# Kernel tuning notes

Hardware: AMD Instinct MI355X
Metric: run time of the kernel (lower is better)

## Reference

```python
import jax, jax.numpy as jnp
import numpy as np

KE = 14.3996454784255
P = 6  # polynomial cutoff order
A_EXP = 0.3
A_PREFACTOR = 0.4543
C = jnp.array([0.1818, 0.5099, 0.2802, 0.02817], dtype=jnp.float32)
K = jnp.array([3.2, 0.9423, 0.4028, 0.2016], dtype=jnp.float32)

N_NODES = 100000
N_EDGES = 6400000
N_ELEM = 10
N_RADII = 119


def setup_inputs() -> dict:
    key = jax.random.key(0)
    k1, k2, k3, k4, k5 = jax.random.split(key, 5)
    # edge distances in a physically plausible range (avoid x ~ 0 -> 1/x blowup)
    x = jax.random.uniform(k1, (N_EDGES, 1), dtype=jnp.float32) * 4.0 + 0.05
    node_attrs = jax.random.uniform(k2, (N_NODES, N_ELEM), dtype=jnp.float32)
    edge_index = jax.random.randint(k3, (2, N_EDGES), 0, N_NODES, dtype=jnp.int64)
    atomic_numbers = jax.random.randint(k4, (N_ELEM,), 1, N_RADII, dtype=jnp.int64)
    # covalent radii table (stand-in for ase.data.covalent_radii), ~0.3..2.6 Angstrom
    covalent_radii = 0.3 + 2.3 * jax.random.uniform(k5, (N_RADII,), dtype=jnp.float32)
    return {
        "x": x,
        "node_attrs": node_attrs,
        "edge_index": edge_index,
        "atomic_numbers": atomic_numbers,
        "covalent_radii": covalent_radii,
    }


def _envelope(x, r_max, p):
    r = x / r_max
    env = (1.0
           - (p + 1.0) * (p + 2.0) / 2.0 * r ** p
           + p * (p + 2.0) * r ** (p + 1)
           - p * (p + 1.0) / 2.0 * r ** (p + 2))
    return env * (x < r_max)


def reference(x, node_attrs, edge_index, atomic_numbers, covalent_radii):
    sender = edge_index[0]    # [E]
    receiver = edge_index[1]  # [E]
    # per-node atomic number from one-hot-ish node_attrs
    node_Z = atomic_numbers[jnp.argmax(node_attrs, axis=1)][:, None]  # [N,1] int
    Z_u = node_Z[sender]   # [E,1] int
    Z_v = node_Z[receiver] # [E,1] int
    Zu_f = Z_u.astype(x.dtype)
    Zv_f = Z_v.astype(x.dtype)
    a = A_PREFACTOR * 0.529 / (Zu_f ** A_EXP + Zv_f ** A_EXP)  # [E,1]
    r_over_a = x / a
    phi = (C[0] * jnp.exp(-K[0] * r_over_a)
           + C[1] * jnp.exp(-K[1] * r_over_a)
           + C[2] * jnp.exp(-K[2] * r_over_a)
           + C[3] * jnp.exp(-K[3] * r_over_a))
    v_edges = KE * Zu_f * Zv_f / x * phi  # [E,1]
    r_max = covalent_radii[Z_u[:, 0]][:, None] + covalent_radii[Z_v[:, 0]][:, None]  # [E,1]
    env = _envelope(x, r_max, float(P))
    v_edges = 0.5 * v_edges * env
    V_ZBL = jax.ops.segment_sum(v_edges, receiver, num_segments=node_attrs.shape[0])  # [N,1]
    return V_ZBL[:, 0]
```

## Files before the change

kernel.cpp:

```cpp
#include <hip/hip_runtime.h>

#define KE_CONST 14.3996454784255f

#define P2_SHIFT 15
#define P2_CHUNK 32768
#define MAXC     4
#define MAXE     16
#define ELEM_CAP 131072
#define CNT_B    256
#define EB       32
#define DN_THR   1024
#define DN_BLOCKS 256
#define SCAN_THR 1024
#define SCAN_B   256

__device__ __forceinline__ void scan_alloc(const unsigned* __restrict__ g_,
        int& nb0, int& nb1, int& nb2, int& nb3,
        int& st1, int& st2, int& st3,
        long long& cs1, long long& cs2, long long& cs3,
        long long& g0, long long& g1, long long& g2, long long& g3) {
    g0 = g_[0]; g1 = g_[1]; g2 = g_[2]; g3 = g_[3];
    long long tot = g0 + g1 + g2 + g3; if (tot < 1) tot = 1;
    nb0 = (int)((g0 * SCAN_B) / tot); if (nb0 < 1) nb0 = 1;
    nb1 = (int)((g1 * SCAN_B) / tot); if (nb1 < 1) nb1 = 1;
    nb2 = (int)((g2 * SCAN_B) / tot); if (nb2 < 1) nb2 = 1;
    nb3 = (int)((g3 * SCAN_B) / tot); if (nb3 < 1) nb3 = 1;
    int sum = nb0 + nb1 + nb2 + nb3;
    while (sum > SCAN_B) {
        if      (nb0 >= nb1 && nb0 >= nb2 && nb0 >= nb3) nb0--;
        else if (nb1 >= nb2 && nb1 >= nb3)               nb1--;
        else if (nb2 >= nb3)                             nb2--;
        else                                             nb3--;
        sum--;
    }
    while (sum < SCAN_B) {
        if      (nb0 >= nb1 && nb0 >= nb2 && nb0 >= nb3) nb0++;
        else if (nb1 >= nb2 && nb1 >= nb3)               nb1++;
        else if (nb2 >= nb3)                             nb2++;
        else                                             nb3++;
        sum++;
    }
    st1 = nb0; st2 = nb0 + nb1; st3 = nb0 + nb1 + nb2;
    cs1 = g0;  cs2 = g0 + g1;   cs3 = g0 + g1 + g2;
}

__device__ __forceinline__ unsigned enc_val16(float xv, const float4& p) {
    float t = xv * p.x;
    float phi = 0.1818f  * __expf(-3.2f    * t)
              + 0.5099f  * __expf(-0.9423f * t)
              + 0.2802f  * __expf(-0.4028f * t)
              + 0.02817f * __expf(-0.2016f * t);
    float rr = xv * p.w;
    float r2 = rr * rr;
    float r6 = r2 * r2 * r2;
    float env = 1.0f - 28.0f * r6 + 48.0f * r6 * rr - 21.0f * r6 * r2;
    float val = fmaxf(p.y * phi / xv * env, 0.0f);
    unsigned e = (__float_as_uint(val) + 0x8000u) >> 16;
    return (xv < p.z) ? e : 0u;
}

__device__ __forceinline__ void scatter_bal(unsigned rw, float xv, const float4& p,
                                            unsigned* cur, const unsigned* seg,
                                            unsigned* __restrict__ packedB, int lane) {
    unsigned cc = rw >> P2_SHIFT;
    unsigned w  = ((rw & (P2_CHUNK - 1)) << 16) | enc_val16(xv, p);
    unsigned long long m0 = __ballot(cc == 0), m1 = __ballot(cc == 1),
                       m2 = __ballot(cc == 2), m3 = __ballot(cc == 3);
    unsigned long long mine = (cc == 0) ? m0 : (cc == 1) ? m1 : (cc == 2) ? m2 : m3;
    int ldr = __ffsll((long long)mine) - 1;
    unsigned base = 0;
    if (lane == ldr) base = atomicAdd(&cur[cc], (unsigned)__popcll(mine));
    base = __shfl(base, ldr, 64);
    unsigned pos = base + (unsigned)__popcll(mine & ((1ull << lane) - 1ull));
    packedB[(size_t)seg[cc] + pos] = w;
}

#define ACC1(W) { if ((W) & 0xFFFFu) \
    atomicAdd(&acc[(W) >> 16], __uint_as_float(((W) & 0xFFFFu) << 16)); }
#define ACC4(Q) { ACC1((Q).x); ACC1((Q).y); ACC1((Q).z); ACC1((Q).w); }

__global__ __launch_bounds__(1024)
void zbl_prep(const float* __restrict__ node_attrs,
              const int* __restrict__ ei,
              const int* __restrict__ atomic_numbers,
              const float* __restrict__ covalent_radii,
              unsigned char* __restrict__ elem_g,
              float4* __restrict__ pair_tab,
              unsigned* __restrict__ gcount,
              unsigned* __restrict__ blkpos,
              int n_edges, int n_elem, int n_nodes) {
    const int b = blockIdx.x, t = threadIdx.x, lane = t & 63;

    if (b < CNT_B) {
        __shared__ unsigned h[MAXC];
        if (t < MAXC) h[t] = 0u;
        __syncthreads();
        long long e0 = (((long long)b * n_edges) / CNT_B) & ~3LL;
        long long e1 = (b == CNT_B - 1) ? (long long)n_edges
                     : ((((long long)(b + 1) * n_edges) / CNT_B) & ~3LL);
        const int* r = ei + n_edges;
        unsigned c0 = 0, c1 = 0, c2 = 0, c3 = 0;
        long long vend = e1 & ~3LL;
        for (long long p = e0 + (long long)t * 4; p + 4 <= vend; p += 1024LL * 4) {
            int4 a = *(const int4*)(r + p);
            unsigned cc;
            cc = ((unsigned)a.x) >> P2_SHIFT; c0 += (cc==0); c1 += (cc==1); c2 += (cc==2); c3 += (cc==3);
            cc = ((unsigned)a.y) >> P2_SHIFT; c0 += (cc==0); c1 += (cc==1); c2 += (cc==2); c3 += (cc==3);
            cc = ((unsigned)a.z) >> P2_SHIFT; c0 += (cc==0); c1 += (cc==1); c2 += (cc==2); c3 += (cc==3);
            cc = ((unsigned)a.w) >> P2_SHIFT; c0 += (cc==0); c1 += (cc==1); c2 += (cc==2); c3 += (cc==3);
        }
        for (long long e2 = vend + t; e2 < e1; e2 += 1024) {
            unsigned cc = ((unsigned)r[e2]) >> P2_SHIFT;
            c0 += (cc==0); c1 += (cc==1); c2 += (cc==2); c3 += (cc==3);
        }
        for (int o = 32; o; o >>= 1) {
            c0 += __shfl_down(c0, o, 64); c1 += __shfl_down(c1, o, 64);
            c2 += __shfl_down(c2, o, 64); c3 += __shfl_down(c3, o, 64);
        }
        if (lane == 0) {
            atomicAdd(&h[0], c0); atomicAdd(&h[1], c1);
            atomicAdd(&h[2], c2); atomicAdd(&h[3], c3);
        }
        __syncthreads();
        if (t < MAXC)
            blkpos[b * MAXC + t] = atomicAdd(&gcount[t], h[t]);
    } else if (b < CNT_B + EB) {
        int bb = b - CNT_B;
        int n0 = (int)(((long long)bb * n_nodes) / EB);
        int n1 = (int)(((long long)(bb + 1) * n_nodes) / EB);
        for (int n = n0 + t; n < n1; n += 1024) {
            const float* row = node_attrs + (size_t)n * n_elem;
            float best = row[0]; int bi = 0;
            for (int i = 1; i < n_elem; ++i) {
                float v = row[i];
                if (v > best) { best = v; bi = i; }
            }
            elem_g[n] = (unsigned char)bi;
        }
    } else {
        int np = n_elem * n_elem;
        if (t < np) {
            int eu = t / n_elem, ev = t - eu * n_elem;
            int Zu = atomic_numbers[eu], Zv = atomic_numbers[ev];
            float zu = (float)Zu, zv = (float)Zv;
            float inv_a = (__powf(zu, 0.3f) + __powf(zv, 0.3f)) * (1.0f / (0.4543f * 0.529f));
            float rmax  = covalent_radii[Zu] + covalent_radii[Zv];
            pair_tab[t] = make_float4(inv_a, 0.5f * KE_CONST * zu * zv, rmax, 1.0f / rmax);
        }
    }
}

__global__ __launch_bounds__(DN_THR)
void zbl_dense(const float* __restrict__ x,
               const int* __restrict__ ei,
               const unsigned char* __restrict__ elem_g,
               const float4* __restrict__ pair_tab,
               const unsigned* __restrict__ gcount,
               const unsigned* __restrict__ blkpos,
               unsigned* __restrict__ packedB,
               int n_edges, int n_elem, int n_nodes) {
    __shared__ __align__(16) unsigned char elem[ELEM_CAP];
    __shared__ float4 pt[MAXE * MAXE];
    __shared__ unsigned cur[MAXC];
    __shared__ unsigned seg[MAXC];

    const int b = blockIdx.x, t = threadIdx.x, lane = t & 63;
    if (t == 0) {
        unsigned G0 = gcount[0], G1 = gcount[1], G2 = gcount[2];
        seg[0] = blkpos[b * MAXC + 0];
        seg[1] = G0 + blkpos[b * MAXC + 1];
        seg[2] = G0 + G1 + blkpos[b * MAXC + 2];
        seg[3] = G0 + G1 + G2 + blkpos[b * MAXC + 3];
        cur[0] = 0; cur[1] = 0; cur[2] = 0; cur[3] = 0;
    }
    int np = n_elem * n_elem;
    for (int i = t; i < np; i += DN_THR) pt[i] = pair_tab[i];
    {
        int nwords = (n_nodes + 15) >> 4;
        const uint4* eg4 = (const uint4*)elem_g;
        uint4* el4 = (uint4*)elem;
        for (int i = t; i < nwords; i += DN_THR) el4[i] = eg4[i];
    }
    __syncthreads();

    long long e0 = (((long long)b * n_edges) / DN_BLOCKS) & ~3LL;
    long long e1 = (b == DN_BLOCKS - 1) ? (long long)n_edges
                 : ((((long long)(b + 1) * n_edges) / DN_BLOCKS) & ~3LL);
    long long vend = e1 & ~3LL;

    for (long long p = e0 + (long long)t * 4; p + 4 <= vend; p += (long long)DN_THR * 4) {
        int4   s4 = *(const int4*)(ei + p);
        int4   r4 = *(const int4*)(ei + n_edges + p);
        float4 x4 = *(const float4*)(x + p);
        float4 p0 = pt[elem[s4.x] * n_elem + elem[r4.x]];
        float4 p1 = pt[elem[s4.y] * n_elem + elem[r4.y]];
        float4 p2 = pt[elem[s4.z] * n_elem + elem[r4.z]];
        float4 p3 = pt[elem[s4.w] * n_elem + elem[r4.w]];
        scatter_bal((unsigned)r4.x, x4.x, p0, cur, seg, packedB, lane);
        scatter_bal((unsigned)r4.y, x4.y, p1, cur, seg, packedB, lane);
        scatter_bal((unsigned)r4.z, x4.z, p2, cur, seg, packedB, lane);
        scatter_bal((unsigned)r4.w, x4.w, p3, cur, seg, packedB, lane);
    }
    for (long long e2 = vend + t; e2 < e1; e2 += DN_THR) {
        int rr = ei[n_edges + e2];
        float4 pp = pt[elem[ei[e2]] * n_elem + elem[rr]];
        scatter_bal((unsigned)rr, x[e2], pp, cur, seg, packedB, lane);
    }
}

__global__ __launch_bounds__(SCAN_THR)
void zbl_scan_bal(const unsigned* __restrict__ packedB,
                  const unsigned* __restrict__ gcount,
                  float* __restrict__ partial) {
    __shared__ __align__(16) float acc[P2_CHUNK];
    const int b = blockIdx.x, t = threadIdx.x;

    int nb0, nb1, nb2, nb3, st1, st2, st3;
    long long cs1, cs2, cs3, g0, g1, g2, g3;
    scan_alloc(gcount, nb0, nb1, nb2, nb3, st1, st2, st3, cs1, cs2, cs3, g0, g1, g2, g3);

    for (int i = t * 4; i < P2_CHUNK; i += SCAN_THR * 4)
        *(float4*)&acc[i] = make_float4(0.f, 0.f, 0.f, 0.f);
    __syncthreads();

    int c   = (b >= st1) + (b >= st2) + (b >= st3);
    int jb  = b - ((c == 0) ? 0 : (c == 1) ? st1 : (c == 2) ? st2 : st3);
    long long gc  = (c == 0) ? g0 : (c == 1) ? g1 : (c == 2) ? g2 : g3;
    int nbc       = (c == 0) ? nb0 : (c == 1) ? nb1 : (c == 2) ? nb2 : nb3;
    long long csc = (c == 0) ? 0LL : (c == 1) ? cs1 : (c == 2) ? cs2 : cs3;
    long long s = csc + gc * jb / nbc;
    long long e = csc + gc * (jb + 1) / nbc;

    long long va = (s + 3) & ~3LL; if (va > e) va = e;
    long long ve = e & ~3LL;       if (ve < va) ve = va;
    for (long long i2 = s + t; i2 < va; i2 += SCAN_THR) { unsigned w = packedB[i2]; ACC1(w); }
    const long long T4 = (long long)SCAN_THR * 4;
    long long niter = (ve - va) / (T4 * 4);
    long long base  = va + (long long)t * 4;
    for (long long it = 0; it < niter; ++it, base += T4 * 4) {
        uint4 q0 = *(const uint4*)(packedB + base);
        uint4 q1 = *(const uint4*)(packedB + base + T4);
        uint4 q2 = *(const uint4*)(packedB + base + 2 * T4);
        uint4 q3 = *(const uint4*)(packedB + base + 3 * T4);
        ACC4(q0); ACC4(q1); ACC4(q2); ACC4(q3);
    }
    long long rem0 = va + niter * T4 * 4;
    for (long long b2 = rem0 + (long long)t * 4; b2 + 4 <= ve; b2 += T4) {
        uint4 q = *(const uint4*)(packedB + b2);
        ACC4(q);
    }
    for (long long i2 = ve + t; i2 < e; i2 += SCAN_THR) { unsigned w = packedB[i2]; ACC1(w); }

    __syncthreads();
    float* pp = partial + (size_t)b * P2_CHUNK;
    for (int i = t * 4; i < P2_CHUNK; i += SCAN_THR * 4)
        *(float4*)(pp + i) = *(const float4*)&acc[i];
}

__global__ void zbl_reduce_bal(const float* __restrict__ partial,
                               const unsigned* __restrict__ gcount,
                               float* __restrict__ out,
                               int n_nodes) {
    int i = blockIdx.x * blockDim.x + threadIdx.x;
    if (i >= n_nodes) return;

    int nb0, nb1, nb2, nb3, st1, st2, st3;
    long long cs1, cs2, cs3, g0, g1, g2, g3;
    scan_alloc(gcount, nb0, nb1, nb2, nb3, st1, st2, st3, cs1, cs2, cs3, g0, g1, g2, g3);

    int c  = i >> P2_SHIFT;
    int li = i & (P2_CHUNK - 1);
    int st  = (c == 0) ? 0 : (c == 1) ? st1 : (c == 2) ? st2 : st3;
    int nbc = (c == 0) ? nb0 : (c == 1) ? nb1 : (c == 2) ? nb2 : nb3;
    const float* p = partial + (size_t)st * P2_CHUNK + li;
    float s0 = 0.f, s1 = 0.f, s2 = 0.f, s3 = 0.f;
    int j = 0;
    for (; j + 4 <= nbc; j += 4) {
        s0 += p[(size_t)(j + 0) * P2_CHUNK];
        s1 += p[(size_t)(j + 1) * P2_CHUNK];
        s2 += p[(size_t)(j + 2) * P2_CHUNK];
        s3 += p[(size_t)(j + 3) * P2_CHUNK];
    }
    for (; j < nbc; ++j) s0 += p[(size_t)j * P2_CHUNK];
    out[i] = (s0 + s1) + (s2 + s3);
}

__global__ void zbl_node_prep(const float* __restrict__ node_attrs,
                              const int* __restrict__ atomic_numbers,
                              const float* __restrict__ covalent_radii,
                              float4* __restrict__ node_data,
                              float* __restrict__ out_zero,
                              int n_nodes, int n_elem) {
    int n = blockIdx.x * blockDim.x + threadIdx.x;
    if (n >= n_nodes) return;
    const float* row = node_attrs + (size_t)n * n_elem;
    float best = row[0];
    int bi = 0;
    for (int i = 1; i < n_elem; ++i) {
        float v = row[i];
        if (v > best) { best = v; bi = i; }
    }
    int Z = atomic_numbers[bi];
    float zf = (float)Z;
    node_data[n] = make_float4(zf, __powf(zf, 0.3f), covalent_radii[Z], 0.0f);
    out_zero[n] = 0.0f;
}

__global__ void zbl_edge_atomic(const float* __restrict__ x,
                                const int* __restrict__ edge_index,
                                const float4* __restrict__ node_data,
                                float* __restrict__ out,
                                int n_edges) {
    int e = blockIdx.x * blockDim.x + threadIdx.x;
    if (e >= n_edges) return;
    int snd = edge_index[e];
    int r = edge_index[n_edges + e];
    float xv = x[e];
    float4 du = node_data[snd];
    float4 dv = node_data[r];
    float rmax = du.z + dv.z;
    if (xv >= rmax) return;
    const float inv_a_pref = 1.0f / (0.4543f * 0.529f);
    float t = xv * (du.y + dv.y) * inv_a_pref;
    float phi = 0.1818f  * __expf(-3.2f    * t)
              + 0.5099f  * __expf(-0.9423f * t)
              + 0.2802f  * __expf(-0.4028f * t)
              + 0.02817f * __expf(-0.2016f * t);
    float v = KE_CONST * du.x * dv.x * phi / xv;
    float rr = xv / rmax;
    float r2 = rr * rr;
    float r6 = r2 * r2 * r2;
    float env = 1.0f - 28.0f * r6 + 48.0f * r6 * rr - 21.0f * r6 * r2;
    atomicAdd(&out[r], 0.5f * v * env);
}

extern "C" void kernel_launch(void* const* d_in, const int* in_sizes, int n_in,
                              void* d_out, int out_size, void* d_ws, size_t ws_size,
                              hipStream_t stream) {
    const float* x              = (const float*)d_in[0];
    const float* node_attrs     = (const float*)d_in[1];
    const int*   edge_index     = (const int*)d_in[2];
    const int*   atomic_numbers = (const int*)d_in[3];
    const float* covalent_radii = (const float*)d_in[4];
    float* out = (float*)d_out;

    int n_edges = in_sizes[0];
    int n_elem  = in_sizes[3];
    int n_nodes = in_sizes[1] / n_elem;

    int C = (n_nodes + P2_CHUNK - 1) >> P2_SHIFT;
    size_t elem_bytes   = (((size_t)n_nodes) + 255) & ~(size_t)255;
    size_t pair_bytes   = ((size_t)MAXE * MAXE * sizeof(float4) + 255) & ~(size_t)255;
    size_t meta_bytes   = (((size_t)(16 + CNT_B * MAXC) * 4) + 255) & ~(size_t)255;
    size_t packed_bytes = (((size_t)n_edges * sizeof(unsigned)) + 255) & ~(size_t)255;
    size_t part_bytes   = (size_t)SCAN_B * P2_CHUNK * sizeof(float);
    bool fast = (C >= 1) && (C <= MAXC) && (n_nodes <= ELEM_CAP) &&
                (n_elem >= 1) && (n_elem <= MAXE) &&
                (ws_size >= elem_bytes + pair_bytes + meta_bytes + packed_bytes + part_bytes);

    if (fast) {
        unsigned char* elem     = (unsigned char*)d_ws;
        float4*        pair_tab = (float4*)((char*)d_ws + elem_bytes);
        unsigned*      gcount   = (unsigned*)((char*)d_ws + elem_bytes + pair_bytes);
        unsigned*      blkpos   = gcount + 16;
        unsigned*      packedB  = (unsigned*)((char*)d_ws + elem_bytes + pair_bytes + meta_bytes);
        float*         part     = (float*)((char*)d_ws + elem_bytes + pair_bytes + meta_bytes + packed_bytes);

        hipMemsetAsync(gcount, 0, 64, stream);

        zbl_prep<<<CNT_B + EB + 1, 1024, 0, stream>>>(
            node_attrs, edge_index, atomic_numbers, covalent_radii,
            elem, pair_tab, gcount, blkpos, n_edges, n_elem, n_nodes);

        zbl_dense<<<DN_BLOCKS, DN_THR, 0, stream>>>(
            x, edge_index, elem, pair_tab, gcount, blkpos, packedB,
            n_edges, n_elem, n_nodes);

        zbl_scan_bal<<<SCAN_B, SCAN_THR, 0, stream>>>(packedB, gcount, part);

        zbl_reduce_bal<<<(n_nodes + 255) / 256, 256, 0, stream>>>(
            part, gcount, out, n_nodes);
        return;
    }

    float4* node_data = (float4*)d_ws;
    zbl_node_prep<<<(n_nodes + 255) / 256, 256, 0, stream>>>(
        node_attrs, atomic_numbers, covalent_radii, node_data,
        out, n_nodes, n_elem);
    zbl_edge_atomic<<<(n_edges + 255) / 256, 256, 0, stream>>>(
        x, edge_index, node_data, out, n_edges);
}
```

Measured before the change: 177.6 us.

## Move bucket counting into dense kernel and replace partial-sum reduction with atomics

The receiver-bucket histogram now runs inside the dense kernel on each block's own edge range, and each block writes its bucketed edges within its own range. This removes the global atomic offset pass and the memset. The scan kernel rebuilds per-bucket prefix sums from the per-block histograms, then walks the matching block segments. It adds its shared-memory totals straight into the output with global float atomics, replacing the 32 MB partial buffer and the separate reduce kernel. In exchange, the edge index is read twice inside the dense kernel, each scan block repeats a small scan, and output atomics make summation order nondeterministic.

```diff
diff --git a/kernel.cpp b/kernel.cpp
--- a/kernel.cpp
+++ b/kernel.cpp
@@ -7,17 +7,15 @@
 #define MAXC     4
 #define MAXE     16
 #define ELEM_CAP 131072
-#define CNT_B    256
-#define EB       32
 #define DN_THR   1024
 #define DN_BLOCKS 256
 #define SCAN_THR 1024
 #define SCAN_B   256
+#define EB       32
 
 __device__ __forceinline__ void scan_alloc(const unsigned* __restrict__ g_,
         int& nb0, int& nb1, int& nb2, int& nb3,
         int& st1, int& st2, int& st3,
-        long long& cs1, long long& cs2, long long& cs3,
         long long& g0, long long& g1, long long& g2, long long& g3) {
     g0 = g_[0]; g1 = g_[1]; g2 = g_[2]; g3 = g_[3];
     long long tot = g0 + g1 + g2 + g3; if (tot < 1) tot = 1;
@@ -41,7 +39,6 @@
         sum++;
     }
     st1 = nb0; st2 = nb0 + nb1; st3 = nb0 + nb1 + nb2;
-    cs1 = g0;  cs2 = g0 + g1;   cs3 = g0 + g1 + g2;
 }
 
 __device__ __forceinline__ unsigned enc_val16(float xv, const float4& p) {
@@ -81,53 +78,16 @@
 
 __global__ __launch_bounds__(1024)
 void zbl_prep(const float* __restrict__ node_attrs,
-              const int* __restrict__ ei,
               const int* __restrict__ atomic_numbers,
               const float* __restrict__ covalent_radii,
               unsigned char* __restrict__ elem_g,
               float4* __restrict__ pair_tab,
-              unsigned* __restrict__ gcount,
-              unsigned* __restrict__ blkpos,
-              int n_edges, int n_elem, int n_nodes) {
-    const int b = blockIdx.x, t = threadIdx.x, lane = t & 63;
-
-    if (b < CNT_B) {
-        __shared__ unsigned h[MAXC];
-        if (t < MAXC) h[t] = 0u;
-        __syncthreads();
-        long long e0 = (((long long)b * n_edges) / CNT_B) & ~3LL;
-        long long e1 = (b == CNT_B - 1) ? (long long)n_edges
-                     : ((((long long)(b + 1) * n_edges) / CNT_B) & ~3LL);
-        const int* r = ei + n_edges;
-        unsigned c0 = 0, c1 = 0, c2 = 0, c3 = 0;
-        long long vend = e1 & ~3LL;
-        for (long long p = e0 + (long long)t * 4; p + 4 <= vend; p += 1024LL * 4) {
-            int4 a = *(const int4*)(r + p);
-            unsigned cc;
-            cc = ((unsigned)a.x) >> P2_SHIFT; c0 += (cc==0); c1 += (cc==1); c2 += (cc==2); c3 += (cc==3);
-            cc = ((unsigned)a.y) >> P2_SHIFT; c0 += (cc==0); c1 += (cc==1); c2 += (cc==2); c3 += (cc==3);
-            cc = ((unsigned)a.z) >> P2_SHIFT; c0 += (cc==0); c1 += (cc==1); c2 += (cc==2); c3 += (cc==3);
-            cc = ((unsigned)a.w) >> P2_SHIFT; c0 += (cc==0); c1 += (cc==1); c2 += (cc==2); c3 += (cc==3);
-        }
-        for (long long e2 = vend + t; e2 < e1; e2 += 1024) {
-            unsigned cc = ((unsigned)r[e2]) >> P2_SHIFT;
-            c0 += (cc==0); c1 += (cc==1); c2 += (cc==2); c3 += (cc==3);
-        }
-        for (int o = 32; o; o >>= 1) {
-            c0 += __shfl_down(c0, o, 64); c1 += __shfl_down(c1, o, 64);
-            c2 += __shfl_down(c2, o, 64); c3 += __shfl_down(c3, o, 64);
-        }
-        if (lane == 0) {
-            atomicAdd(&h[0], c0); atomicAdd(&h[1], c1);
-            atomicAdd(&h[2], c2); atomicAdd(&h[3], c3);
-        }
-        __syncthreads();
-        if (t < MAXC)
-            blkpos[b * MAXC + t] = atomicAdd(&gcount[t], h[t]);
-    } else if (b < CNT_B + EB) {
-        int bb = b - CNT_B;
-        int n0 = (int)(((long long)bb * n_nodes) / EB);
-        int n1 = (int)(((long long)(bb + 1) * n_nodes) / EB);
+              float* __restrict__ out,
+              int n_elem, int n_nodes) {
+    const int b = blockIdx.x, t = threadIdx.x;
+    if (b < EB) {
+        int n0 = (int)(((long long)b * n_nodes) / EB);
+        int n1 = (int)(((long long)(b + 1) * n_nodes) / EB);
         for (int n = n0 + t; n < n1; n += 1024) {
             const float* row = node_attrs + (size_t)n * n_elem;
             float best = row[0]; int bi = 0;
@@ -136,6 +96,7 @@
                 if (v > best) { best = v; bi = i; }
             }
             elem_g[n] = (unsigned char)bi;
+            out[n] = 0.0f;
         }
     } else {
         int np = n_elem * n_elem;
@@ -155,24 +116,56 @@
                const int* __restrict__ ei,
                const unsigned char* __restrict__ elem_g,
                const float4* __restrict__ pair_tab,
-               const unsigned* __restrict__ gcount,
-               const unsigned* __restrict__ blkpos,
+               unsigned* __restrict__ hist,
                unsigned* __restrict__ packedB,
                int n_edges, int n_elem, int n_nodes) {
     __shared__ __align__(16) unsigned char elem[ELEM_CAP];
     __shared__ float4 pt[MAXE * MAXE];
-    __shared__ unsigned cur[MAXC];
-    __shared__ unsigned seg[MAXC];
+    __shared__ unsigned mh[MAXC], cur[MAXC], seg[MAXC];
 
     const int b = blockIdx.x, t = threadIdx.x, lane = t & 63;
+    long long e0 = (((long long)b * n_edges) / DN_BLOCKS) & ~3LL;
+    long long e1 = (b == DN_BLOCKS - 1) ? (long long)n_edges
+                 : ((((long long)(b + 1) * n_edges) / DN_BLOCKS) & ~3LL);
+    long long vend = e1 & ~3LL;
+
+    if (t < MAXC) mh[t] = 0u;
+    __syncthreads();
+
+    {
+        const int* r = ei + n_edges;
+        unsigned c0 = 0, c1 = 0, c2 = 0, c3 = 0;
+        for (long long p = e0 + (long long)t * 4; p + 4 <= vend; p += (long long)DN_THR * 4) {
+            int4 a = *(const int4*)(r + p);
+            unsigned cc;
+            cc = ((unsigned)a.x) >> P2_SHIFT; c0 += (cc==0); c1 += (cc==1); c2 += (cc==2); c3 += (cc==3);
+            cc = ((unsigned)a.y) >> P2_SHIFT; c0 += (cc==0); c1 += (cc==1); c2 += (cc==2); c3 += (cc==3);
+            cc = ((unsigned)a.z) >> P2_SHIFT; c0 += (cc==0); c1 += (cc==1); c2 += (cc==2); c3 += (cc==3);
+            cc = ((unsigned)a.w) >> P2_SHIFT; c0 += (cc==0); c1 += (cc==1); c2 += (cc==2); c3 += (cc==3);
+        }
+        for (long long e2 = vend + t; e2 < e1; e2 += DN_THR) {
+            unsigned cc = ((unsigned)r[e2]) >> P2_SHIFT;
+            c0 += (cc==0); c1 += (cc==1); c2 += (cc==2); c3 += (cc==3);
+        }
+        for (int o = 32; o; o >>= 1) {
+            c0 += __shfl_down(c0, o, 64); c1 += __shfl_down(c1, o, 64);
+            c2 += __shfl_down(c2, o, 64); c3 += __shfl_down(c3, o, 64);
+        }
+        if (lane == 0) {
+            atomicAdd(&mh[0], c0); atomicAdd(&mh[1], c1);
+            atomicAdd(&mh[2], c2); atomicAdd(&mh[3], c3);
+        }
+    }
+    __syncthreads();
     if (t == 0) {
-        unsigned G0 = gcount[0], G1 = gcount[1], G2 = gcount[2];
-        seg[0] = blkpos[b * MAXC + 0];
-        seg[1] = G0 + blkpos[b * MAXC + 1];
-        seg[2] = G0 + G1 + blkpos[b * MAXC + 2];
-        seg[3] = G0 + G1 + G2 + blkpos[b * MAXC + 3];
+        seg[0] = (unsigned)e0;
+        seg[1] = seg[0] + mh[0];
+        seg[2] = seg[1] + mh[1];
+        seg[3] = seg[2] + mh[2];
         cur[0] = 0; cur[1] = 0; cur[2] = 0; cur[3] = 0;
     }
+    if (t < MAXC) hist[b * MAXC + t] = mh[t];
+
     int np = n_elem * n_elem;
     for (int i = t; i < np; i += DN_THR) pt[i] = pair_tab[i];
     {
@@ -182,11 +175,6 @@
         for (int i = t; i < nwords; i += DN_THR) el4[i] = eg4[i];
     }
     __syncthreads();
-
-    long long e0 = (((long long)b * n_edges) / DN_BLOCKS) & ~3LL;
-    long long e1 = (b == DN_BLOCKS - 1) ? (long long)n_edges
-                 : ((((long long)(b + 1) * n_edges) / DN_BLOCKS) & ~3LL);
-    long long vend = e1 & ~3LL;
 
     for (long long p = e0 + (long long)t * 4; p + 4 <= vend; p += (long long)DN_THR * 4) {
         int4   s4 = *(const int4*)(ei + p);
@@ -209,80 +197,88 @@
 }
 
 __global__ __launch_bounds__(SCAN_THR)
-void zbl_scan_bal(const unsigned* __restrict__ packedB,
-                  const unsigned* __restrict__ gcount,
-                  float* __restrict__ partial) {
+void zbl_scan_d(const unsigned* __restrict__ packedB,
+                const unsigned* __restrict__ hist,
+                float* __restrict__ out,
+                int n_edges, int n_nodes) {
     __shared__ __align__(16) float acc[P2_CHUNK];
+    __shared__ unsigned h_lds[DN_BLOCKS * MAXC];
+    __shared__ unsigned sb[MAXC * DN_BLOCKS];
+    __shared__ unsigned tot[MAXC];
     const int b = blockIdx.x, t = threadIdx.x;
 
-    int nb0, nb1, nb2, nb3, st1, st2, st3;
-    long long cs1, cs2, cs3, g0, g1, g2, g3;
-    scan_alloc(gcount, nb0, nb1, nb2, nb3, st1, st2, st3, cs1, cs2, cs3, g0, g1, g2, g3);
-
+    for (int i = t; i < DN_BLOCKS * MAXC; i += SCAN_THR) h_lds[i] = hist[i];
     for (int i = t * 4; i < P2_CHUNK; i += SCAN_THR * 4)
         *(float4*)&acc[i] = make_float4(0.f, 0.f, 0.f, 0.f);
     __syncthreads();
 
-    int c   = (b >= st1) + (b >= st2) + (b >= st3);
-    int jb  = b - ((c == 0) ? 0 : (c == 1) ? st1 : (c == 2) ? st2 : st3);
-    long long gc  = (c == 0) ? g0 : (c == 1) ? g1 : (c == 2) ? g2 : g3;
+    {
+        const int c = t >> 8, bb = t & 255;
+        sb[t] = h_lds[bb * MAXC + c];
+        __syncthreads();
+        for (int off = 1; off < DN_BLOCKS; off <<= 1) {
+            unsigned add = (bb >= off) ? sb[c * DN_BLOCKS + bb - off] : 0u;
+            __syncthreads();
+            sb[t] += add;
+            __syncthreads();
+        }
+        if (bb == 255) tot[c] = sb[t];
+    }
+    __syncthreads();
+
+    int nb0, nb1, nb2, nb3, st1, st2, st3;
+    long long g0, g1, g2, g3;
+    scan_alloc(tot, nb0, nb1, nb2, nb3, st1, st2, st3, g0, g1, g2, g3);
+
+    const int c   = (b >= st1) + (b >= st2) + (b >= st3);
+    const int jb  = b - ((c == 0) ? 0 : (c == 1) ? st1 : (c == 2) ? st2 : st3);
+    long long Tc  = (c == 0) ? g0 : (c == 1) ? g1 : (c == 2) ? g2 : g3;
     int nbc       = (c == 0) ? nb0 : (c == 1) ? nb1 : (c == 2) ? nb2 : nb3;
-    long long csc = (c == 0) ? 0LL : (c == 1) ? cs1 : (c == 2) ? cs2 : cs3;
-    long long s = csc + gc * jb / nbc;
-    long long e = csc + gc * (jb + 1) / nbc;
-
-    long long va = (s + 3) & ~3LL; if (va > e) va = e;
-    long long ve = e & ~3LL;       if (ve < va) ve = va;
-    for (long long i2 = s + t; i2 < va; i2 += SCAN_THR) { unsigned w = packedB[i2]; ACC1(w); }
-    const long long T4 = (long long)SCAN_THR * 4;
-    long long niter = (ve - va) / (T4 * 4);
-    long long base  = va + (long long)t * 4;
-    for (long long it = 0; it < niter; ++it, base += T4 * 4) {
-        uint4 q0 = *(const uint4*)(packedB + base);
-        uint4 q1 = *(const uint4*)(packedB + base + T4);
-        uint4 q2 = *(const uint4*)(packedB + base + 2 * T4);
-        uint4 q3 = *(const uint4*)(packedB + base + 3 * T4);
-        ACC4(q0); ACC4(q1); ACC4(q2); ACC4(q3);
-    }
-    long long rem0 = va + niter * T4 * 4;
-    for (long long b2 = rem0 + (long long)t * 4; b2 + 4 <= ve; b2 += T4) {
-        uint4 q = *(const uint4*)(packedB + b2);
-        ACC4(q);
-    }
-    for (long long i2 = ve + t; i2 < e; i2 += SCAN_THR) { unsigned w = packedB[i2]; ACC1(w); }
-
-    __syncthreads();
-    float* pp = partial + (size_t)b * P2_CHUNK;
-    for (int i = t * 4; i < P2_CHUNK; i += SCAN_THR * 4)
-        *(float4*)(pp + i) = *(const float4*)&acc[i];
-}
-
-__global__ void zbl_reduce_bal(const float* __restrict__ partial,
-                               const unsigned* __restrict__ gcount,
-                               float* __restrict__ out,
-                               int n_nodes) {
-    int i = blockIdx.x * blockDim.x + threadIdx.x;
-    if (i >= n_nodes) return;
-
-    int nb0, nb1, nb2, nb3, st1, st2, st3;
-    long long cs1, cs2, cs3, g0, g1, g2, g3;
-    scan_alloc(gcount, nb0, nb1, nb2, nb3, st1, st2, st3, cs1, cs2, cs3, g0, g1, g2, g3);
-
-    int c  = i >> P2_SHIFT;
-    int li = i & (P2_CHUNK - 1);
-    int st  = (c == 0) ? 0 : (c == 1) ? st1 : (c == 2) ? st2 : st3;
-    int nbc = (c == 0) ? nb0 : (c == 1) ? nb1 : (c == 2) ? nb2 : nb3;
-    const float* p = partial + (size_t)st * P2_CHUNK + li;
-    float s0 = 0.f, s1 = 0.f, s2 = 0.f, s3 = 0.f;
-    int j = 0;
-    for (; j + 4 <= nbc; j += 4) {
-        s0 += p[(size_t)(j + 0) * P2_CHUNK];
-        s1 += p[(size_t)(j + 1) * P2_CHUNK];
-        s2 += p[(size_t)(j + 2) * P2_CHUNK];
-        s3 += p[(size_t)(j + 3) * P2_CHUNK];
-    }
-    for (; j < nbc; ++j) s0 += p[(size_t)j * P2_CHUNK];
-    out[i] = (s0 + s1) + (s2 + s3);
+    long long w0 = Tc * jb / nbc;
+    long long w1 = Tc * (jb + 1) / nbc;
+
+    if (w0 < w1) {
+        int lo = 0, hi = DN_BLOCKS;
+        while (lo < hi) {
+            int mid = (lo + hi) >> 1;
+            if ((long long)sb[c * DN_BLOCKS + mid] > w0) hi = mid; else lo = mid + 1;
+        }
+        int bb = lo;
+        long long w = w0;
+        while (w < w1 && bb < DN_BLOCKS) {
+            long long excl = (bb == 0) ? 0LL : (long long)sb[c * DN_BLOCKS + bb - 1];
+            unsigned hbc = h_lds[bb * MAXC + c];
+            long long pe = excl + hbc; if (pe > w1) pe = w1;
+            if (pe > w) {
+                long long eb0 = (((long long)bb * n_edges) / DN_BLOCKS) & ~3LL;
+                unsigned segoff = 0;
+                for (int cc2 = 0; cc2 < c; ++cc2) segoff += h_lds[bb * MAXC + cc2];
+                long long gs = eb0 + segoff + (w - excl);
+                long long ge = gs + (pe - w);
+                long long gva = (gs + 3) & ~3LL; if (gva > ge) gva = ge;
+                long long gve = ge & ~3LL;       if (gve < gva) gve = gva;
+                for (long long i2 = gs + t; i2 < gva; i2 += SCAN_THR) {
+                    unsigned wd = packedB[i2]; ACC1(wd);
+                }
+                for (long long i2 = gva + (long long)t * 4; i2 < gve; i2 += (long long)SCAN_THR * 4) {
+                    uint4 q = *(const uint4*)(packedB + i2);
+                    ACC4(q);
+                }
+                for (long long i2 = gve + t; i2 < ge; i2 += SCAN_THR) {
+                    unsigned wd = packedB[i2]; ACC1(wd);
+                }
+            }
+            w = pe; ++bb;
+        }
+    }
+
+    __syncthreads();
+    long long nodebase = (long long)c << P2_SHIFT;
+    for (int i = t; i < P2_CHUNK; i += SCAN_THR) {
+        float v = acc[i];
+        if (v != 0.0f && nodebase + i < n_nodes)
+            atomicAdd(&out[nodebase + i], v);
+    }
 }
 
 __global__ void zbl_node_prep(const float* __restrict__ node_attrs,
@@ -351,35 +347,28 @@
     int C = (n_nodes + P2_CHUNK - 1) >> P2_SHIFT;
     size_t elem_bytes   = (((size_t)n_nodes) + 255) & ~(size_t)255;
     size_t pair_bytes   = ((size_t)MAXE * MAXE * sizeof(float4) + 255) & ~(size_t)255;
-    size_t meta_bytes   = (((size_t)(16 + CNT_B * MAXC) * 4) + 255) & ~(size_t)255;
+    size_t hist_bytes   = (((size_t)DN_BLOCKS * MAXC * 4) + 255) & ~(size_t)255;
     size_t packed_bytes = (((size_t)n_edges * sizeof(unsigned)) + 255) & ~(size_t)255;
-    size_t part_bytes   = (size_t)SCAN_B * P2_CHUNK * sizeof(float);
     bool fast = (C >= 1) && (C <= MAXC) && (n_nodes <= ELEM_CAP) &&
                 (n_elem >= 1) && (n_elem <= MAXE) &&
-                (ws_size >= elem_bytes + pair_bytes + meta_bytes + packed_bytes + part_bytes);
+                (ws_size >= elem_bytes + pair_bytes + hist_bytes + packed_bytes);
 
     if (fast) {
         unsigned char* elem     = (unsigned char*)d_ws;
         float4*        pair_tab = (float4*)((char*)d_ws + elem_bytes);
-        unsigned*      gcount   = (unsigned*)((char*)d_ws + elem_bytes + pair_bytes);
-        unsigned*      blkpos   = gcount + 16;
-        unsigned*      packedB  = (unsigned*)((char*)d_ws + elem_bytes + pair_bytes + meta_bytes);
-        float*         part     = (float*)((char*)d_ws + elem_bytes + pair_bytes + meta_bytes + packed_bytes);
-
-        hipMemsetAsync(gcount, 0, 64, stream);
-
-        zbl_prep<<<CNT_B + EB + 1, 1024, 0, stream>>>(
-            node_attrs, edge_index, atomic_numbers, covalent_radii,
-            elem, pair_tab, gcount, blkpos, n_edges, n_elem, n_nodes);
+        unsigned*      hist     = (unsigned*)((char*)d_ws + elem_bytes + pair_bytes);
+        unsigned*      packedB  = (unsigned*)((char*)d_ws + elem_bytes + pair_bytes + hist_bytes);
+
+        zbl_prep<<<EB + 1, 1024, 0, stream>>>(
+            node_attrs, atomic_numbers, covalent_radii,
+            elem, pair_tab, out, n_elem, n_nodes);
 
         zbl_dense<<<DN_BLOCKS, DN_THR, 0, stream>>>(
-            x, edge_index, elem, pair_tab, gcount, blkpos, packedB,
+            x, edge_index, elem, pair_tab, hist, packedB,
             n_edges, n_elem, n_nodes);
 
-        zbl_scan_bal<<<SCAN_B, SCAN_THR, 0, stream>>>(packedB, gcount, part);
-
-        zbl_reduce_bal<<<(n_nodes + 255) / 256, 256, 0, stream>>>(
-            part, gcount, out, n_nodes);
+        zbl_scan_d<<<SCAN_B, SCAN_THR, 0, stream>>>(
+            packedB, hist, out, n_edges, n_nodes);
         return;
     }
 
```

Result: slower. 228.2 us (+28.5%).
